# Optimization experiments

Measured on AMD Instinct MI355X. Metric: run time of the kernel, lower is better.

## Reference

```python
import jax, jax.numpy as jnp
import numpy as np


def setup_inputs() -> dict:
    key = jax.random.key(0)
    k1, _ = jax.random.split(key)
    x = jax.random.normal(k1, (8, 128, 56, 56), dtype=jnp.float32)
    gamma = jnp.array(0.5, dtype=jnp.float32)  # learned scalar (init gamma=0.5)
    return {"x": x, "gamma": gamma}


def reference(x, gamma):
    # conv=False path: query/key/value convs are Identity, so Q=K=V=x flattened.
    B, C, H, W = x.shape
    N = H * W
    v = x.reshape(B, C, N)                          # [B, C, N]
    # energy[b, i, j] = sum_c x[b, c, i] * x[b, c, j]  (Q^T K)
    energy = jnp.einsum('bci,bcj->bij', v, v)       # [B, N, N]
    # multiplicative mask: zero out the diagonal BEFORE softmax (not -inf)
    mask = 1.0 - jnp.eye(N, dtype=energy.dtype)
    attention = jax.nn.softmax(energy * mask, axis=-1)  # [B, N, N]
    # out = bmm(V, attention): out[b, c, j] = sum_i v[b, c, i] * attention[b, i, j]
    out = jnp.einsum('bci,bij->bcj', v, attention)  # [B, C, N]
    out = jax.nn.relu(out).reshape(B, C, H, W)
    y = gamma * out + x
    return (y, out, x, gamma)
```

## Files before the change

### kernel.cpp

```cpp
#include <hip/hip_runtime.h>
#include <math.h>

#define Bb 8
#define Cc 128
#define Nn 3136
#define Np 3200
#define Mm (Bb*Cc*Nn)
#define PADX 136
#define PADV 72
#define SHIFT 44.0f

typedef unsigned short u16;
typedef unsigned int   u32;
typedef __attribute__((ext_vector_type(8)))  u16      u16x8;
typedef __attribute__((ext_vector_type(8)))  _Float16 f16x8;
typedef __attribute__((ext_vector_type(4)))  _Float16 f16x4;
typedef __attribute__((ext_vector_type(4)))  float    f32x4;
typedef __attribute__((ext_vector_type(16))) float    f32x16;

__global__ __launch_bounds__(256) void prep_kernel(const float* __restrict__ x,
                                                   const float* __restrict__ gamma_p,
                                                   float* __restrict__ out,
                                                   u16* __restrict__ xt,
                                                   u16* __restrict__ xc,
                                                   float* __restrict__ row_d) {
    const int bx = blockIdx.x;
    const int b = bx / 50, nblk = bx % 50;
    const int t = threadIdx.x;

    if (nblk == 49) {
        const u16x8 z8 = {0, 0, 0, 0, 0, 0, 0, 0};
        #pragma unroll
        for (int it = 0; it < 4; ++it) {
            const int idx = it * 256 + t, row = idx / 17, seg = idx % 17;
            *(u16x8*)&xt[(size_t)(b * Np + Nn + row) * PADX + seg * 8] = z8;
        }
        if (t < 64) {
            const int idx = 1024 + t, row = idx / 17, seg = idx % 17;
            *(u16x8*)&xt[(size_t)(b * Np + Nn + row) * PADX + seg * 8] = z8;
        }
        #pragma unroll
        for (int it = 0; it < 4; ++it) {
            const int idx = it * 256 + t, c = idx >> 3, seg = idx & 7;
            *(u16x8*)&xc[(size_t)(b * Cc + c) * Np + Nn + seg * 8] = z8;
        }
        if (t < 64) row_d[b * Np + Nn + t] = 1.0f;
        return;
    }

    __shared__ float lx[Cc][65];
    const int n0 = nblk * 64;

    #pragma unroll 8
    for (int r = 0; r < 32; ++r) {
        const int c = r * 4 + (t >> 6);
        const int g = (b * Cc + c) * Nn + n0 + (t & 63);
        const float v = x[g];
        lx[c][t & 63] = v;
        out[(size_t)2 * Mm + g] = v;
    }
    __syncthreads();

    {
        const int nl = t & 63, cseg = t >> 6;
        u16x8 hv[4];
        #pragma unroll
        for (int cc = 0; cc < 32; ++cc) {
            const _Float16 hh = (_Float16)lx[cseg * 32 + cc][nl];
            hv[cc >> 3][cc & 7] = __builtin_bit_cast(u16, hh);
        }
        const size_t base = (size_t)(b * Np + n0 + nl) * PADX + cseg * 32;
        #pragma unroll
        for (int k = 0; k < 4; ++k) *(u16x8*)&xt[base + k * 8] = hv[k];
    }
    {
        const int c = t >> 1, half = t & 1;
        u16x8 hv[4];
        #pragma unroll
        for (int k = 0; k < 32; ++k) {
            const _Float16 hh = (_Float16)lx[c][half * 32 + k];
            hv[k >> 3][k & 7] = __builtin_bit_cast(u16, hh);
        }
        const size_t base = (size_t)(b * Cc + c) * Np + n0 + half * 32;
        #pragma unroll
        for (int k = 0; k < 4; ++k) *(u16x8*)&xc[base + k * 8] = hv[k];
    }
    if (bx == 0 && t == 0) out[(size_t)3 * Mm] = gamma_p[0];
}

__global__ __launch_bounds__(256, 3) void stats_kernel(const u16* __restrict__ xt,
                                                       float* __restrict__ row_d) {
    __shared__ u16 s_jt[64 * PADX];

    const int bx = blockIdx.x;
    const int b = bx / 98, rem = bx % 98;
    const int i0 = (rem >> 1) * 64, jh = rem & 1;
    const int t = threadIdx.x;
    const int w = t >> 6, l = t & 63, lane = l & 31, h = l >> 5;
    const int igrp = w & 1, jsub = w >> 1;

    f16x8 Bf[8];
    {
        const size_t rb = (size_t)(b * Np + i0 + igrp * 32 + lane) * PADX + h * 8;
        #pragma unroll
        for (int kk = 0; kk < 8; ++kk)
            Bf[kk] = *(const f16x8*)&xt[rb + kk * 16];
    }

    float sa = 0.0f, sb = 0.0f;
    const int jt0 = jh * 25;

    for (int jt = jt0; jt < jt0 + 25; ++jt) {
        const int j0 = jt * 64;
        __syncthreads();
        {
            const u16* src = xt + (size_t)(b * Np + j0) * PADX;
            u16x8 tv[4], tv4;
            #pragma unroll
            for (int it = 0; it < 4; ++it)
                tv[it] = *(const u16x8*)&src[(it * 256 + t) * 8];
            if (t < 64) tv4 = *(const u16x8*)&src[(1024 + t) * 8];
            #pragma unroll
            for (int it = 0; it < 4; ++it)
                *(u16x8*)&s_jt[(it * 256 + t) * 8] = tv[it];
            if (t < 64) *(u16x8*)&s_jt[(1024 + t) * 8] = tv4;
        }
        __syncthreads();

        f32x16 ea, eb;
        #pragma unroll
        for (int r = 0; r < 16; ++r) { ea[r] = 0.0f; eb[r] = 0.0f; }
        const int arow = (jsub * 32 + lane) * PADX + h * 8;
        #pragma unroll
        for (int kk = 0; kk < 4; ++kk) {
            const f16x8 A0 = *(const f16x8*)&s_jt[arow + (2 * kk) * 16];
            const f16x8 A1 = *(const f16x8*)&s_jt[arow + (2 * kk + 1) * 16];
            ea = __builtin_amdgcn_mfma_f32_32x32x16_f16(A0, Bf[2 * kk], ea, 0, 0, 0);
            eb = __builtin_amdgcn_mfma_f32_32x32x16_f16(A1, Bf[2 * kk + 1], eb, 0, 0, 0);
        }

        const bool diag = (j0 == i0) && (jsub == igrp);
        #pragma unroll
        for (int r = 0; r < 16; ++r) {
            const int mrow = (r & 3) + 8 * (r >> 2) + 4 * h;
            float v = ea[r] + eb[r];
            if (diag && (mrow == lane)) v = 0.0f;
            if (r & 1) sb += __expf(v - SHIFT); else sa += __expf(v - SHIFT);
        }
    }

    float ssum = sa + sb;
    ssum += __shfl_xor(ssum, 32, 64);
    if (h == 0) atomicAdd(&row_d[b * Np + i0 + igrp * 32 + lane], ssum);
}

__global__ __launch_bounds__(256, 3) void out_kernel(const float* __restrict__ x,
                                                     const u16* __restrict__ xt,
                                                     const u16* __restrict__ xc,
                                                     const float* __restrict__ row_d,
                                                     const float* __restrict__ gamma_p,
                                                     float* __restrict__ out) {
    __shared__ u16 s_xt[64 * PADX];
    __shared__ u16 s_xc[Cc * PADV];
    __shared__ u16 s_pt[64 * PADV];

    const int bx = blockIdx.x;
    const int b = bx / 49, j0 = (bx % 49) * 64;
    const int t = threadIdx.x;
    const int w = t >> 6, l = t & 63, lane = l & 31, h = l >> 5;
    const int isub = w & 1, jgrp = w >> 1;
    const int jg = w & 1,  cp = w >> 1;
    const u16* __restrict__ xtb = xt + (size_t)b * Np * PADX;
    const u16* __restrict__ xcb = xc + (size_t)b * Cc * Np;

    f16x8 Bj[8];
    {
        const size_t rb = (size_t)(j0 + jgrp * 32 + lane) * PADX + h * 8;
        #pragma unroll
        for (int kk = 0; kk < 8; ++kk)
            Bj[kk] = *(const f16x8*)&xtb[rb + kk * 16];
    }

    f32x16 oa, ob;
    #pragma unroll
    for (int r = 0; r < 16; ++r) { oa[r] = 0.0f; ob[r] = 0.0f; }

    for (int ti = 0; ti < 50; ++ti) {
        const int i0g = ti * 64;
        __syncthreads();
        {
            const u16* srct = xtb + (size_t)i0g * PADX;
            u16x8 vt[4], vt4, vcr[4];
            #pragma unroll
            for (int it = 0; it < 4; ++it) {
                vt[it] = *(const u16x8*)&srct[(it * 256 + t) * 8];
                const int q = it * 256 + t;
                vcr[it] = *(const u16x8*)&xcb[(size_t)(q >> 3) * Np + i0g + (q & 7) * 8];
            }
            if (t < 64) vt4 = *(const u16x8*)&srct[(1024 + t) * 8];
            #pragma unroll
            for (int it = 0; it < 4; ++it) {
                *(u16x8*)&s_xt[(it * 256 + t) * 8] = vt[it];
                const int q = it * 256 + t;
                *(u16x8*)&s_xc[(q >> 3) * PADV + (q & 7) * 8] = vcr[it];
            }
            if (t < 64) *(u16x8*)&s_xt[(1024 + t) * 8] = vt4;
        }
        __syncthreads();

        f32x16 ea, eb;
        #pragma unroll
        for (int r = 0; r < 16; ++r) { ea[r] = 0.0f; eb[r] = 0.0f; }
        const int arow = (isub * 32 + lane) * PADX + h * 8;
        #pragma unroll
        for (int kk = 0; kk < 4; ++kk) {
            const f16x8 A0 = *(const f16x8*)&s_xt[arow + (2 * kk) * 16];
            const f16x8 A1 = *(const f16x8*)&s_xt[arow + (2 * kk + 1) * 16];
            ea = __builtin_amdgcn_mfma_f32_32x32x16_f16(A0, Bj[2 * kk], ea, 0, 0, 0);
            eb = __builtin_amdgcn_mfma_f32_32x32x16_f16(A1, Bj[2 * kk + 1], eb, 0, 0, 0);
        }

        const bool mayDiag = (j0 < i0g + 64) && (i0g < j0 + 64);
        const int ptbase = (jgrp * 32 + lane) * PADV + isub * 32;
        #pragma unroll
        for (int q = 0; q < 4; ++q) {
            const f32x4 dq = *(const f32x4*)&row_d[b * Np + i0g + isub * 32 + q * 8 + h * 4];
            f16x4 pv;
            #pragma unroll
            for (int r = 0; r < 4; ++r) {
                const int m = q * 8 + h * 4 + r;
                float v = ea[q * 4 + r] + eb[q * 4 + r];
                if (mayDiag && (i0g + isub * 32 + m == j0 + jgrp * 32 + lane)) v = 0.0f;
                pv[r] = (_Float16)(__expf(v - SHIFT) * __builtin_amdgcn_rcpf(dq[r]));
            }
            *(f16x4*)&s_pt[ptbase + q * 8 + h * 4] = pv;
        }
        __syncthreads();

        const int pbrow = (jg * 32 + lane) * PADV + h * 8;
        const int va0 = (cp * 64 + lane) * PADV + h * 8;
        const int va1 = va0 + 32 * PADV;
        #pragma unroll
        for (int kk = 0; kk < 4; ++kk) {
            const f16x8 Bp  = *(const f16x8*)&s_pt[pbrow + kk * 16];
            const f16x8 Av0 = *(const f16x8*)&s_xc[va0 + kk * 16];
            const f16x8 Av1 = *(const f16x8*)&s_xc[va1 + kk * 16];
            oa = __builtin_amdgcn_mfma_f32_32x32x16_f16(Av0, Bp, oa, 0, 0, 0);
            ob = __builtin_amdgcn_mfma_f32_32x32x16_f16(Av1, Bp, ob, 0, 0, 0);
        }
    }

    const float gamma = gamma_p[0];
    #pragma unroll
    for (int r = 0; r < 16; ++r) {
        const int mrow = (r & 3) + 8 * (r >> 2) + 4 * h;
        const int jj = j0 + jg * 32 + lane;
        {
            const int c = cp * 64 + mrow;
            const size_t pos = (size_t)(b * Cc + c) * Nn + jj;
            const float o = fmaxf(oa[r], 0.0f);
            out[pos] = fmaf(gamma, o, x[pos]);
            out[(size_t)Mm + pos] = o;
        }
        {
            const int c = cp * 64 + 32 + mrow;
            const size_t pos = (size_t)(b * Cc + c) * Nn + jj;
            const float o = fmaxf(ob[r], 0.0f);
            out[pos] = fmaf(gamma, o, x[pos]);
            out[(size_t)Mm + pos] = o;
        }
    }
}

extern "C" void kernel_launch(void* const* d_in, const int* in_sizes, int n_in,
                              void* d_out, int out_size, void* d_ws, size_t ws_size,
                              hipStream_t stream) {
    const float* x       = (const float*)d_in[0];
    const float* gamma_p = (const float*)d_in[1];
    float* out = (float*)d_out;

    float* row_d = (float*)d_ws;
    u16* xt = (u16*)((char*)d_ws + (1 << 17));
    u16* xc = xt + (size_t)Bb * Np * PADX;

    hipMemsetAsync(row_d, 0, (size_t)Bb * Np * sizeof(float), stream);
    prep_kernel <<<400, 256, 0, stream>>>(x, gamma_p, out, xt, xc, row_d);
    stats_kernel<<<784, 256, 0, stream>>>(xt, row_d);
    out_kernel  <<<392, 256, 0, stream>>>(x, xt, xc, row_d, gamma_p, out);
}
```

Measured before the change: 204.8 us.

## Split out_kernel key range across two blocks and add reduce pass; use exp2

The attention-output kernel now splits the i (key) loop into two halves, launching twice as many blocks. Each half writes partial sums into the two output slots, and a new reduce kernel adds them, applies relu and the gamma residual. Separately, x is prescaled by sqrt(log2 e) before fp16 conversion so softmax can use the hardware exp2 directly instead of __expf. This raises occupancy and parallelism for the 392-block kernel at the cost of an extra kernel launch and additional global memory traffic; the prescale slightly changes fp16 rounding.

```diff
diff --git a/kernel.cpp b/kernel.cpp
--- a/kernel.cpp
+++ b/kernel.cpp
@@ -8,7 +8,10 @@
 #define Mm (Bb*Cc*Nn)
 #define PADX 136
 #define PADV 72
-#define SHIFT 44.0f
+#define SHIFT2 63.4785818f
+#define SSCALE 1.2011224087f
+
+#define EXP2F(v) __builtin_amdgcn_exp2f(v)
 
 typedef unsigned short u16;
 typedef unsigned int   u32;
@@ -66,7 +69,7 @@
         u16x8 hv[4];
         #pragma unroll
         for (int cc = 0; cc < 32; ++cc) {
-            const _Float16 hh = (_Float16)lx[cseg * 32 + cc][nl];
+            const _Float16 hh = (_Float16)(lx[cseg * 32 + cc][nl] * SSCALE);
             hv[cc >> 3][cc & 7] = __builtin_bit_cast(u16, hh);
         }
         const size_t base = (size_t)(b * Np + n0 + nl) * PADX + cseg * 32;
@@ -145,7 +148,7 @@
             const int mrow = (r & 3) + 8 * (r >> 2) + 4 * h;
             float v = ea[r] + eb[r];
             if (diag && (mrow == lane)) v = 0.0f;
-            if (r & 1) sb += __expf(v - SHIFT); else sa += __expf(v - SHIFT);
+            if (r & 1) sb += EXP2F(v - SHIFT2); else sa += EXP2F(v - SHIFT2);
         }
     }
 
@@ -154,18 +157,17 @@
     if (h == 0) atomicAdd(&row_d[b * Np + i0 + igrp * 32 + lane], ssum);
 }
 
-__global__ __launch_bounds__(256, 3) void out_kernel(const float* __restrict__ x,
-                                                     const u16* __restrict__ xt,
+__global__ __launch_bounds__(256, 3) void out_kernel(const u16* __restrict__ xt,
                                                      const u16* __restrict__ xc,
                                                      const float* __restrict__ row_d,
-                                                     const float* __restrict__ gamma_p,
                                                      float* __restrict__ out) {
     __shared__ u16 s_xt[64 * PADX];
     __shared__ u16 s_xc[Cc * PADV];
     __shared__ u16 s_pt[64 * PADV];
 
     const int bx = blockIdx.x;
-    const int b = bx / 49, j0 = (bx % 49) * 64;
+    const int b = bx / 98, rem = bx % 98;
+    const int j0 = (rem >> 1) * 64, half = rem & 1;
     const int t = threadIdx.x;
     const int w = t >> 6, l = t & 63, lane = l & 31, h = l >> 5;
     const int isub = w & 1, jgrp = w >> 1;
@@ -185,8 +187,8 @@
     #pragma unroll
     for (int r = 0; r < 16; ++r) { oa[r] = 0.0f; ob[r] = 0.0f; }
 
-    for (int ti = 0; ti < 50; ++ti) {
-        const int i0g = ti * 64;
+    for (int ti = 0; ti < 25; ++ti) {
+        const int i0g = (half * 25 + ti) * 64;
         __syncthreads();
         {
             const u16* srct = xtb + (size_t)i0g * PADX;
@@ -231,7 +233,7 @@
                 const int m = q * 8 + h * 4 + r;
                 float v = ea[q * 4 + r] + eb[q * 4 + r];
                 if (mayDiag && (i0g + isub * 32 + m == j0 + jgrp * 32 + lane)) v = 0.0f;
-                pv[r] = (_Float16)(__expf(v - SHIFT) * __builtin_amdgcn_rcpf(dq[r]));
+                pv[r] = (_Float16)(EXP2F(v - SHIFT2) * __builtin_amdgcn_rcpf(dq[r]));
             }
             *(f16x4*)&s_pt[ptbase + q * 8 + h * 4] = pv;
         }
@@ -250,25 +252,37 @@
         }
     }
 
-    const float gamma = gamma_p[0];
+    float* __restrict__ slotp = out + (size_t)half * Mm;
     #pragma unroll
     for (int r = 0; r < 16; ++r) {
         const int mrow = (r & 3) + 8 * (r >> 2) + 4 * h;
         const int jj = j0 + jg * 32 + lane;
-        {
-            const int c = cp * 64 + mrow;
-            const size_t pos = (size_t)(b * Cc + c) * Nn + jj;
-            const float o = fmaxf(oa[r], 0.0f);
-            out[pos] = fmaf(gamma, o, x[pos]);
-            out[(size_t)Mm + pos] = o;
-        }
-        {
-            const int c = cp * 64 + 32 + mrow;
-            const size_t pos = (size_t)(b * Cc + c) * Nn + jj;
-            const float o = fmaxf(ob[r], 0.0f);
-            out[pos] = fmaf(gamma, o, x[pos]);
-            out[(size_t)Mm + pos] = o;
-        }
+        slotp[(size_t)(b * Cc + cp * 64 + mrow) * Nn + jj] = oa[r];
+        slotp[(size_t)(b * Cc + cp * 64 + 32 + mrow) * Nn + jj] = ob[r];
+    }
+}
+
+__global__ __launch_bounds__(256) void reduce_kernel(const float* __restrict__ x,
+                                                     const float* __restrict__ gamma_p,
+                                                     float* __restrict__ out) {
+    const float gamma = gamma_p[0];
+    float* __restrict__ s0 = out;
+    float* __restrict__ s1 = out + (size_t)Mm;
+    const size_t base = (size_t)blockIdx.x * 4096 + threadIdx.x * 4;
+    #pragma unroll
+    for (int it = 0; it < 4; ++it) {
+        const size_t k = base + it * 1024;
+        const f32x4 p0 = *(const f32x4*)&s0[k];
+        const f32x4 p1 = *(const f32x4*)&s1[k];
+        const f32x4 xv = *(const f32x4*)&x[k];
+        f32x4 o, y;
+        #pragma unroll
+        for (int r = 0; r < 4; ++r) {
+            o[r] = fmaxf(p0[r] + p1[r], 0.0f);
+            y[r] = fmaf(gamma, o[r], xv[r]);
+        }
+        *(f32x4*)&s0[k] = y;
+        *(f32x4*)&s1[k] = o;
     }
 }
 
@@ -283,8 +297,9 @@
     u16* xt = (u16*)((char*)d_ws + (1 << 17));
     u16* xc = xt + (size_t)Bb * Np * PADX;
 
-    hipMemsetAsync(row_d, 0, (size_t)Bb * Np * sizeof(float), stream);
-    prep_kernel <<<400, 256, 0, stream>>>(x, gamma_p, out, xt, xc, row_d);
-    stats_kernel<<<784, 256, 0, stream>>>(xt, row_d);
-    out_kernel  <<<392, 256, 0, stream>>>(x, xt, xc, row_d, gamma_p, out);
-}
+    (void)hipMemsetAsync(row_d, 0, (size_t)Bb * Np * sizeof(float), stream);
+    prep_kernel  <<<400, 256, 0, stream>>>(x, gamma_p, out, xt, xc, row_d);
+    stats_kernel <<<784, 256, 0, stream>>>(xt, row_d);
+    out_kernel   <<<784, 256, 0, stream>>>(xt, xc, row_d, out);
+    reduce_kernel<<<784, 256, 0, stream>>>(x, gamma_p, out);
+}
```

Result: slower. 209.7 us (+2.4%).
